# Kernel optimization log

Hardware: AMD Instinct MI355X
Metric: run time of the kernel (lower is better)

The kernel has to match this reference:

```python
import jax, jax.numpy as jnp
import numpy as np

B, S, DIM, H = 2, 2048, 1024, 16
DK = DIM // H  # 64
NEG = -10000000000.0


def setup_inputs() -> dict:
    key = jax.random.key(0)
    k1, k2, k3, k4, k5, k6 = jax.random.split(key, 6)
    dec_xs = jax.random.normal(k1, (B, S, DIM), dtype=jnp.float32)
    enc_xs = jax.random.normal(k2, (B, S, DIM), dtype=jnp.float32)
    mask = jax.random.randint(k3, (B, S, S), 0, 2, dtype=jnp.int32)
    # torch Linear weights: out = x @ W.T, bias=False
    sc = 1.0 / np.sqrt(DIM)
    Wq = jax.random.normal(k4, (DIM, DIM), dtype=jnp.float32) * sc
    Wkv = jax.random.normal(k5, (2 * DIM, DIM), dtype=jnp.float32) * sc
    Wo = jax.random.normal(k6, (DIM, DIM), dtype=jnp.float32) * sc
    return {"dec_xs": dec_xs, "enc_xs": enc_xs, "Wq": Wq, "Wkv": Wkv, "Wo": Wo, "mask": mask}


def reference(dec_xs, enc_xs, Wq, Wkv, Wo, mask):
    b, s, dim = enc_xs.shape
    qs = dec_xs @ Wq.T                      # [b,s,dim]  (dropout inactive in eval)
    kv = enc_xs @ Wkv.T                     # [b,s,2*dim]
    ks, vs = jnp.split(kv, 2, axis=-1)
    # head layout: view(b, s, dk, h) -- heads LAST, as in the original
    qs = qs.reshape(b, s, DK, H)
    ks = ks.reshape(b, s, DK, H)
    vs = vs.reshape(b, s, DK, H)
    scores = jnp.einsum('bqdh,bkdh->bqkh', qs, ks) / np.sqrt(DK)
    scores = jnp.where(mask[..., None] == 0, NEG, scores)
    weights = jax.nn.softmax(scores, axis=-2)  # softmax over key axis
    out = jnp.einsum('bqkh,bkdh->bqdh', weights, vs).reshape(b, s, dim)
    return out @ Wo.T
```

## Files before the change

kernel.cpp:

```cpp
#include <hip/hip_runtime.h>
#include <hip/hip_bf16.h>

#define BB 2
#define SS 2048
#define DIMM 1024
#define HH 16
#define DKK 64
#define QSCALE 0.18033688011112042592f

using bf16 = __hip_bfloat16;
typedef __attribute__((ext_vector_type(8))) short v8s;
typedef __attribute__((ext_vector_type(4))) short v4s;
typedef __attribute__((ext_vector_type(4))) float f32x4;
typedef __attribute__((ext_vector_type(16))) float f32x16;

using lds_u32 = __attribute__((address_space(3))) unsigned int;
using glb_u32 = const __attribute__((address_space(1))) unsigned int;

__device__ __forceinline__ void gload16(void* lds, const void* g) {
  __builtin_amdgcn_global_load_lds((glb_u32*)g, (lds_u32*)lds, 16, 0, 0);
}

__device__ __forceinline__ void cvt4(const float* __restrict__ s,
                                     bf16* __restrict__ d, int idx) {
  const float4 f = ((const float4*)s)[idx];
  bf16 t[4] = {__float2bfloat16(f.x), __float2bfloat16(f.y),
               __float2bfloat16(f.z), __float2bfloat16(f.w)};
  *(v4s*)(d + (size_t)idx * 4) = *(const v4s*)t;
}

__device__ __forceinline__ int cvt_pk_bf16(float lo, float hi) {
  int r;
  asm("v_cvt_pk_bf16_f32 %0, %1, %2" : "=v"(r) : "v"(lo), "v"(hi));
  return r;
}

__global__ __launch_bounds__(256) void convert_pack_kernel(
    const float* __restrict__ dec, const float* __restrict__ enc,
    const float* __restrict__ Wq, const float* __restrict__ Wkv,
    const float* __restrict__ Wo, const int* __restrict__ mask,
    bf16* __restrict__ decb, bf16* __restrict__ encb, bf16* __restrict__ Wqb,
    bf16* __restrict__ Wkvb, bf16* __restrict__ Wob,
    unsigned long long* __restrict__ mp) {
  const int gid = blockIdx.x * 256 + threadIdx.x;
  const int NT = 256 * 1024;
#pragma unroll
  for (int i = 0; i < 4; ++i) cvt4(dec, decb, gid + i * NT);
#pragma unroll
  for (int i = 0; i < 4; ++i) cvt4(enc, encb, gid + i * NT);
  cvt4(Wq, Wqb, gid);
#pragma unroll
  for (int i = 0; i < 2; ++i) cvt4(Wkv, Wkvb, gid + i * NT);
  {
    const int n = gid >> 8;
    const int c4 = (gid & 255) * 4;
    const int h = c4 >> 6, d0 = c4 & 63;
    const float* src = Wo + (size_t)n * DIMM + h;
    bf16 t[4];
#pragma unroll
    for (int i2 = 0; i2 < 4; ++i2)
      t[i2] = __float2bfloat16(src[(d0 + i2) * 16]);
    *(v4s*)(Wob + (size_t)n * DIMM + c4) = *(const v4s*)t;
  }
  const int lane = threadIdx.x & 63;
  const int wave_id = gid >> 6;
  for (int i = 0; i < 32; ++i) {
    const size_t w = (size_t)wave_id * 32 + i;
    const unsigned long long bm = __ballot(mask[w * 64 + lane] != 0);
    if (lane == 0) {
      const int bb = (int)(w >> 16);
      const int qq = (int)((w >> 5) & 2047);
      const int kc = (int)(w & 31);
      mp[((size_t)bb * 32 + kc) * SS + qq] = bm;
    }
  }
}

__global__ __launch_bounds__(256) void proj_gemm_kernel(
    const bf16* __restrict__ decb, const bf16* __restrict__ encb,
    const bf16* __restrict__ Wqb, const bf16* __restrict__ Wkvb,
    bf16* __restrict__ Qr, bf16* __restrict__ Kr, bf16* __restrict__ Vt) {
  __shared__ __align__(16) bf16 As[2][128][64];
  __shared__ __align__(16) bf16 Bs[2][128][64];
  const int t = threadIdx.x;
  const int wave = t >> 6, lane = t & 63;
  const int quad = lane >> 4, l15 = lane & 15;
  const int wm = (wave >> 1) * 64, wn = (wave & 1) * 64;

  const int bid = blockIdx.x;
  const int xcd = bid & 7, slot = bid >> 3;
  const int km = xcd + 8 * (slot >> 3);
  const int g = slot & 7;
  const int kind = km >> 5;
  const int m0 = (km & 31) * 128;

  const int lrow = lane >> 3;
  const int lcol = (lane & 7) * 8;

  const bf16* aptr[4];
  const bf16* bptr[4];
#pragma unroll
  for (int j = 0; j < 4; ++j) {
    const int r = (wave * 4 + j) * 8 + lrow;
    const int pw = (r & 63) * 16 + g * 2 + (r >> 6);
    if (kind == 0) {
      aptr[j] = decb + (size_t)(m0 + r) * DIMM + lcol;
      bptr[j] = Wqb + (size_t)pw * DIMM + lcol;
    } else if (kind == 1) {
      aptr[j] = encb + (size_t)(m0 + r) * DIMM + lcol;
      bptr[j] = Wkvb + (size_t)pw * DIMM + lcol;
    } else {
      aptr[j] = Wkvb + (size_t)(pw + DIMM) * DIMM + lcol;
      bptr[j] = encb + (size_t)(m0 + r) * DIMM + lcol;
    }
  }

  auto stage = [&](int kc, int buf) {
#pragma unroll
    for (int j = 0; j < 4; ++j) {
      gload16(&As[buf][(wave * 4 + j) * 8][0], aptr[j] + kc);
      gload16(&Bs[buf][(wave * 4 + j) * 8][0], bptr[j] + kc);
    }
  };

  f32x4 acc[4][4] = {};
  stage(0, 0);

  for (int kt = 0; kt < 16; ++kt) {
    const int cb = kt & 1;
    __syncthreads();
    if (kt < 15) stage((kt + 1) * 64, cb ^ 1);
#pragma unroll
    for (int ks = 0; ks < 2; ++ks) {
      v8s af[4], bfr[4];
#pragma unroll
      for (int i = 0; i < 4; ++i)
        af[i] = *(const v8s*)&As[cb][wm + i * 16 + l15][ks * 32 + quad * 8];
#pragma unroll
      for (int j = 0; j < 4; ++j)
        bfr[j] = *(const v8s*)&Bs[cb][wn + j * 16 + l15][ks * 32 + quad * 8];
#pragma unroll
      for (int i = 0; i < 4; ++i)
#pragma unroll
        for (int j = 0; j < 4; ++j)
          acc[i][j] = __builtin_amdgcn_mfma_f32_16x16x32_bf16(
              af[i], bfr[j], acc[i][j], 0, 0, 0);
    }
  }

#pragma unroll
  for (int i = 0; i < 4; ++i) {
#pragma unroll
    for (int r = 0; r < 4; ++r) {
      const int mm = wm + i * 16 + quad * 4 + r;
#pragma unroll
      for (int j = 0; j < 4; ++j) {
        const int nn = wn + j * 16 + l15;
        const float v = acc[i][j][r];
        if (kind == 0) {
          Qr[(size_t)(m0 + mm) * DIMM + g * 128 + nn] =
              __float2bfloat16(v * QSCALE);
        } else if (kind == 1) {
          Kr[(size_t)(m0 + mm) * DIMM + g * 128 + nn] = __float2bfloat16(v);
        } else {
          const int h = g * 2 + (mm >> 6), d = mm & 63;
          const int sn = m0 + nn;
          const int b = sn >> 11, s = sn & (SS - 1);
          Vt[(((size_t)b * HH + h) * DKK + d) * SS + s] = __float2bfloat16(v);
        }
      }
    }
  }
}

__global__ __launch_bounds__(256) void out_gemm_kernel(
    const bf16* __restrict__ A, const bf16* __restrict__ W,
    float* __restrict__ out) {
  __shared__ __align__(16) bf16 As[2][128][64];
  __shared__ __align__(16) bf16 Bs[2][128][64];
  const int t = threadIdx.x;
  const int wave = t >> 6, lane = t & 63;
  const int quad = lane >> 4, l15 = lane & 15;
  const int wm = (wave >> 1) * 64, wn = (wave & 1) * 64;

  const int bid = blockIdx.x;
  const int xcd = bid & 7, slot = bid >> 3;
  const int m0 = (xcd + 8 * (slot >> 3)) * 128;
  const int n0 = (slot & 7) * 128;

  const int lrow = lane >> 3;
  const int lcol = (lane & 7) * 8;

  const bf16* aptr[4];
  const bf16* bptr[4];
#pragma unroll
  for (int j = 0; j < 4; ++j) {
    const int r = (wave * 4 + j) * 8 + lrow;
    aptr[j] = A + (size_t)(m0 + r) * DIMM + lcol;
    bptr[j] = W + (size_t)(n0 + r) * DIMM + lcol;
  }

  auto stage = [&](int kc, int buf) {
#pragma unroll
    for (int j = 0; j < 4; ++j) {
      gload16(&As[buf][(wave * 4 + j) * 8][0], aptr[j] + kc);
      gload16(&Bs[buf][(wave * 4 + j) * 8][0], bptr[j] + kc);
    }
  };

  f32x4 acc[4][4] = {};
  stage(0, 0);

  for (int kt = 0; kt < 16; ++kt) {
    const int cb = kt & 1;
    __syncthreads();
    if (kt < 15) stage((kt + 1) * 64, cb ^ 1);
#pragma unroll
    for (int ks = 0; ks < 2; ++ks) {
      v8s af[4], bfr[4];
#pragma unroll
      for (int i = 0; i < 4; ++i)
        af[i] = *(const v8s*)&As[cb][wm + i * 16 + l15][ks * 32 + quad * 8];
#pragma unroll
      for (int j = 0; j < 4; ++j)
        bfr[j] = *(const v8s*)&Bs[cb][wn + j * 16 + l15][ks * 32 + quad * 8];
#pragma unroll
      for (int i = 0; i < 4; ++i)
#pragma unroll
        for (int j = 0; j < 4; ++j)
          acc[i][j] = __builtin_amdgcn_mfma_f32_16x16x32_bf16(
              af[i], bfr[j], acc[i][j], 0, 0, 0);
    }
  }

#pragma unroll
  for (int i = 0; i < 4; ++i) {
#pragma unroll
    for (int r = 0; r < 4; ++r) {
      const int m = m0 + wm + i * 16 + quad * 4 + r;
#pragma unroll
      for (int j = 0; j < 4; ++j) {
        const int n = n0 + wn + j * 16 + l15;
        out[(size_t)m * DIMM + n] = acc[i][j][r];
      }
    }
  }
}

__global__ __launch_bounds__(512) void attn_kernel(
    const bf16* __restrict__ Qr, const bf16* __restrict__ Kr,
    const bf16* __restrict__ Vt, const unsigned long long* __restrict__ mp,
    bf16* __restrict__ Ar) {
  __shared__ __align__(16) bf16 smem[2][2][2][64][72];

  const int t = threadIdx.x;
  const int wave = t >> 6, lane = t & 63;
  const int l31 = lane & 31, hf = lane >> 5;
  const int qb = wave & 3;
  const int pr = wave >> 2;

  const int bx = blockIdx.x;
  const int xcd = bx & 7, j = bx >> 3;
  const int g = (xcd << 2) | (j & 3);
  const int tile = j >> 2;
  const int hd = g & 15, b = g >> 4;

  const int qw = tile * 128 + qb * 32;
  const size_t bhv = ((size_t)b * HH + hd) * DKK;

  v8s bq[4];
  {
    const bf16* qrow = Qr + ((size_t)(b * SS + qw + l31)) * DIMM + hd * 64;
#pragma unroll
    for (int cs = 0; cs < 4; ++cs)
      bq[cs] = *(const v8s*)(qrow + cs * 16 + 8 * hf);
  }

  v8s vones;
#pragma unroll
  for (int i = 0; i < 8; ++i) vones[i] = (short)0x3F80;

  f32x16 o0 = {}, o1 = {}, ol = {};

  const int r0 = t >> 3;
  const int c0 = (t & 7) * 8;

  auto gK = [&](int kt) {
    return *(const v8s*)(Kr + ((size_t)(b * SS + kt * 64 + r0)) * DIMM +
                         hd * 64 + c0);
  };
  auto gV = [&](int kt) {
    return *(const v8s*)(Vt + (bhv + r0) * SS + kt * 64 + c0);
  };
  auto loadM = [&](int kt) {
    return mp[((size_t)b * 32 + kt) * SS + qw + l31];
  };

  {
    const v8s k0 = gK(0), v0 = gV(0), k1 = gK(1), v1 = gV(1);
    *(v8s*)&smem[0][0][0][r0][c0] = k0;
    *(v8s*)&smem[1][0][0][r0][c0] = v0;
    *(v8s*)&smem[0][1][0][r0][c0] = k1;
    *(v8s*)&smem[1][1][0][r0][c0] = v1;
  }
  v8s kpr[2], vpr[2];
  kpr[0] = gK(2);
  vpr[0] = gV(2);
  kpr[1] = gK(3);
  vpr[1] = gV(3);
  unsigned long long mwcur = loadM(pr);

  for (int s = 0; s < 16; ++s) {
    __syncthreads();
    const int nb = (s + 1) & 1;
    if (s < 15) {
      *(v8s*)&smem[0][0][nb][r0][c0] = kpr[0];
      *(v8s*)&smem[1][0][nb][r0][c0] = vpr[0];
      *(v8s*)&smem[0][1][nb][r0][c0] = kpr[1];
      *(v8s*)&smem[1][1][nb][r0][c0] = vpr[1];
      if (s < 14) {
        kpr[0] = gK(2 * s + 4);
        vpr[0] = gV(2 * s + 4);
        kpr[1] = gK(2 * s + 5);
        vpr[1] = gV(2 * s + 5);
      }
    }
    const unsigned long long mwnext = (s < 15) ? loadM(2 * s + 2 + pr) : 0ULL;
    const unsigned long long mq = mwcur >> (4 * hf);
    const int cb = s & 1;

    f32x16 st[2];
#pragma unroll
    for (int n = 0; n < 2; ++n) {
      f32x16 sa = {};
#pragma unroll
      for (int cs = 0; cs < 4; ++cs) {
        const v8s ak =
            *(const v8s*)&smem[0][pr][cb][n * 32 + l31][cs * 16 + 8 * hf];
        sa = __builtin_amdgcn_mfma_f32_32x32x16_bf16(ak, bq[cs], sa, 0, 0, 0);
      }
      st[n] = sa;
    }

    int pd[8][2];
#pragma unroll
    for (int n = 0; n < 2; ++n)
#pragma unroll
      for (int g2 = 0; g2 < 4; ++g2)
#pragma unroll
        for (int jj = 0; jj < 2; ++jj) {
          const int bp = 32 * n + 8 * g2 + 2 * jj;
          const int m = g2 * 4 + 2 * jj;
          const float p0 =
              ((mq >> bp) & 1) ? __builtin_amdgcn_exp2f(st[n][m]) : 0.f;
          const float p1 =
              ((mq >> (bp + 1)) & 1) ? __builtin_amdgcn_exp2f(st[n][m + 1])
                                     : 0.f;
          pd[n * 4 + g2][jj] = cvt_pk_bf16(p0, p1);
        }

    v8s af[4];
#pragma unroll
    for (int ks = 0; ks < 4; ++ks) {
      int a0 = pd[2 * ks][0], b0 = pd[2 * ks + 1][0];
      int a1 = pd[2 * ks][1], b1 = pd[2 * ks + 1][1];
      asm("v_permlane32_swap_b32 %0, %1" : "+v"(a0), "+v"(b0));
      asm("v_permlane32_swap_b32 %0, %1" : "+v"(a1), "+v"(b1));
      int4 w;
      w.x = a0;
      w.y = a1;
      w.z = b0;
      w.w = b1;
      af[ks] = *(v8s*)&w;
    }

#pragma unroll
    for (int ks = 0; ks < 4; ++ks) {
      const v8s bv0 = *(const v8s*)&smem[1][pr][cb][l31][ks * 16 + 8 * hf];
      const v8s bv1 =
          *(const v8s*)&smem[1][pr][cb][32 + l31][ks * 16 + 8 * hf];
      o0 = __builtin_amdgcn_mfma_f32_32x32x16_bf16(af[ks], bv0, o0, 0, 0, 0);
      o1 = __builtin_amdgcn_mfma_f32_32x32x16_bf16(af[ks], bv1, o1, 0, 0, 0);
      ol = __builtin_amdgcn_mfma_f32_32x32x16_bf16(af[ks], vones, ol, 0, 0, 0);
    }
    mwcur = mwnext;
  }

  __syncthreads();
  float* scratch = (float*)&smem[0][0][0][0][0];
  if (wave >= 4) {
    float* dst = scratch + ((size_t)(wave - 4) * 64 + lane) * 52;
#pragma unroll
    for (int i = 0; i < 4; ++i) {
      f32x4 t0 = {o0[4 * i], o0[4 * i + 1], o0[4 * i + 2], o0[4 * i + 3]};
      f32x4 t1 = {o1[4 * i], o1[4 * i + 1], o1[4 * i + 2], o1[4 * i + 3]};
      f32x4 t2 = {ol[4 * i], ol[4 * i + 1], ol[4 * i + 2], ol[4 * i + 3]};
      *(f32x4*)(dst + 4 * i) = t0;
      *(f32x4*)(dst + 16 + 4 * i) = t1;
      *(f32x4*)(dst + 32 + 4 * i) = t2;
    }
  }
  __syncthreads();
  if (wave < 4) {
    const float* src = scratch + ((size_t)wave * 64 + lane) * 52;
#pragma unroll
    for (int m = 0; m < 16; ++m) {
      o0[m] += src[m];
      o1[m] += src[16 + m];
      ol[m] += src[32 + m];
    }
#pragma unroll
    for (int m = 0; m < 16; ++m) {
      const float inv = __builtin_amdgcn_rcpf(ol[m]);
      const int q = qw + (m & 3) + 8 * (m >> 2) + 4 * hf;
      const size_t row = (size_t)b * SS + q;
      Ar[row * DIMM + hd * 64 + l31] = __float2bfloat16(o0[m] * inv);
      Ar[row * DIMM + hd * 64 + 32 + l31] = __float2bfloat16(o1[m] * inv);
    }
  }
}

extern "C" void kernel_launch(void* const* d_in, const int* in_sizes, int n_in,
                              void* d_out, int out_size, void* d_ws,
                              size_t ws_size, hipStream_t stream) {
  const float* dec = (const float*)d_in[0];
  const float* enc = (const float*)d_in[1];
  const float* Wq = (const float*)d_in[2];
  const float* Wkv = (const float*)d_in[3];
  const float* Wo = (const float*)d_in[4];
  const int* mask = (const int*)d_in[5];
  float* out = (float*)d_out;

  bf16* decb = (bf16*)d_out;
  bf16* Wqb = (bf16*)((char*)d_out + ((size_t)2 * SS * DIMM * 2));

  char* ws = (char*)d_ws;
  size_t off = 0;
  bf16* encb = (bf16*)(ws + off);
  bf16* Ar = (bf16*)(ws + off);   off += (size_t)2 * SS * DIMM * 2;
  bf16* Wkvb = (bf16*)(ws + off); off += (size_t)2 * DIMM * DIMM * 2;
  bf16* Wob = (bf16*)(ws + off);  off += (size_t)DIMM * DIMM * 2;
  bf16* Qr = (bf16*)(ws + off);   off += (size_t)2 * SS * DIMM * 2;
  bf16* Kr = (bf16*)(ws + off);   off += (size_t)2 * SS * DIMM * 2;
  bf16* Vt = (bf16*)(ws + off);   off += (size_t)2 * SS * DIMM * 2;
  unsigned long long* mp = (unsigned long long*)(ws + off);

  dim3 blk(256);
  convert_pack_kernel<<<dim3(1024), blk, 0, stream>>>(
      dec, enc, Wq, Wkv, Wo, mask, decb, encb, Wqb, Wkvb, Wob, mp);
  proj_gemm_kernel<<<dim3(768), blk, 0, stream>>>(decb, encb, Wqb, Wkvb, Qr,
                                                  Kr, Vt);
  attn_kernel<<<dim3(512), dim3(512), 0, stream>>>(Qr, Kr, Vt, mp, Ar);
  out_gemm_kernel<<<dim3(256), blk, 0, stream>>>(Ar, Wob, out);
}
```

Before: 268.2 us.

## Swizzle proj GEMM LDS layout and retile output GEMM to 128x64 padded tiles

Result: faster. 242.4 us (-9.6%).

```diff
diff --git a/kernel.cpp b/kernel.cpp
--- a/kernel.cpp
+++ b/kernel.cpp
@@ -95,7 +95,7 @@
   const int m0 = (km & 31) * 128;
 
   const int lrow = lane >> 3;
-  const int lcol = (lane & 7) * 8;
+  const int lcol = ((lane & 7) ^ lrow) * 8;
 
   const bf16* aptr[4];
   const bf16* bptr[4];
@@ -132,13 +132,14 @@
     if (kt < 15) stage((kt + 1) * 64, cb ^ 1);
 #pragma unroll
     for (int ks = 0; ks < 2; ++ks) {
+      const int rc = (((ks * 4 + quad) ^ (l15 & 7)) * 8);
       v8s af[4], bfr[4];
 #pragma unroll
       for (int i = 0; i < 4; ++i)
-        af[i] = *(const v8s*)&As[cb][wm + i * 16 + l15][ks * 32 + quad * 8];
+        af[i] = *(const v8s*)&As[cb][wm + i * 16 + l15][rc];
 #pragma unroll
       for (int j = 0; j < 4; ++j)
-        bfr[j] = *(const v8s*)&Bs[cb][wn + j * 16 + l15][ks * 32 + quad * 8];
+        bfr[j] = *(const v8s*)&Bs[cb][wn + j * 16 + l15][rc];
 #pragma unroll
       for (int i = 0; i < 4; ++i)
 #pragma unroll
@@ -176,58 +177,66 @@
 __global__ __launch_bounds__(256) void out_gemm_kernel(
     const bf16* __restrict__ A, const bf16* __restrict__ W,
     float* __restrict__ out) {
-  __shared__ __align__(16) bf16 As[2][128][64];
-  __shared__ __align__(16) bf16 Bs[2][128][64];
+  __shared__ __align__(16) bf16 As[128][72];
+  __shared__ __align__(16) bf16 Bs[64][72];
   const int t = threadIdx.x;
   const int wave = t >> 6, lane = t & 63;
   const int quad = lane >> 4, l15 = lane & 15;
-  const int wm = (wave >> 1) * 64, wn = (wave & 1) * 64;
+  const int wm = (wave >> 1) * 64, wn = (wave & 1) * 32;
 
   const int bid = blockIdx.x;
   const int xcd = bid & 7, slot = bid >> 3;
-  const int m0 = (xcd + 8 * (slot >> 3)) * 128;
-  const int n0 = (slot & 7) * 128;
-
-  const int lrow = lane >> 3;
-  const int lcol = (lane & 7) * 8;
-
-  const bf16* aptr[4];
-  const bf16* bptr[4];
-#pragma unroll
-  for (int j = 0; j < 4; ++j) {
-    const int r = (wave * 4 + j) * 8 + lrow;
-    aptr[j] = A + (size_t)(m0 + r) * DIMM + lcol;
-    bptr[j] = W + (size_t)(n0 + r) * DIMM + lcol;
-  }
-
-  auto stage = [&](int kc, int buf) {
-#pragma unroll
-    for (int j = 0; j < 4; ++j) {
-      gload16(&As[buf][(wave * 4 + j) * 8][0], aptr[j] + kc);
-      gload16(&Bs[buf][(wave * 4 + j) * 8][0], bptr[j] + kc);
-    }
-  };
-
-  f32x4 acc[4][4] = {};
-  stage(0, 0);
-
-  for (int kt = 0; kt < 16; ++kt) {
-    const int cb = kt & 1;
+  const int m0 = (xcd + 8 * (slot >> 4)) * 128;
+  const int n0 = (slot & 15) * 64;
+
+  const int sr = t >> 2;
+  const int sc = (t & 3) * 16;
+
+  v8s ar[4], br[2];
+  auto loadA = [&](int kc) {
+#pragma unroll
+    for (int rr = 0; rr < 2; ++rr) {
+      const bf16* p = A + (size_t)(m0 + sr + rr * 64) * DIMM + kc + sc;
+#pragma unroll
+      for (int i = 0; i < 2; ++i) ar[rr * 2 + i] = ((const v8s*)p)[i];
+    }
+  };
+  auto loadB = [&](int kc) {
+    const bf16* p = W + (size_t)(n0 + sr) * DIMM + kc + sc;
+#pragma unroll
+    for (int i = 0; i < 2; ++i) br[i] = ((const v8s*)p)[i];
+  };
+
+  f32x4 acc[4][2] = {};
+  loadA(0);
+  loadB(0);
+  for (int kc = 0; kc < DIMM; kc += 64) {
     __syncthreads();
-    if (kt < 15) stage((kt + 1) * 64, cb ^ 1);
+#pragma unroll
+    for (int rr = 0; rr < 2; ++rr) {
+      *(v8s*)&As[sr + rr * 64][sc] = ar[rr * 2 + 0];
+      *(v8s*)&As[sr + rr * 64][sc + 8] = ar[rr * 2 + 1];
+    }
+    *(v8s*)&Bs[sr][sc] = br[0];
+    *(v8s*)&Bs[sr][sc + 8] = br[1];
+    if (kc + 64 < DIMM) {
+      loadA(kc + 64);
+      loadB(kc + 64);
+    }
+    __syncthreads();
 #pragma unroll
     for (int ks = 0; ks < 2; ++ks) {
-      v8s af[4], bfr[4];
+      v8s af[4], bfr[2];
 #pragma unroll
       for (int i = 0; i < 4; ++i)
-        af[i] = *(const v8s*)&As[cb][wm + i * 16 + l15][ks * 32 + quad * 8];
-#pragma unroll
-      for (int j = 0; j < 4; ++j)
-        bfr[j] = *(const v8s*)&Bs[cb][wn + j * 16 + l15][ks * 32 + quad * 8];
+        af[i] = *(const v8s*)&As[wm + i * 16 + l15][ks * 32 + quad * 8];
+#pragma unroll
+      for (int j = 0; j < 2; ++j)
+        bfr[j] = *(const v8s*)&Bs[wn + j * 16 + l15][ks * 32 + quad * 8];
 #pragma unroll
       for (int i = 0; i < 4; ++i)
 #pragma unroll
-        for (int j = 0; j < 4; ++j)
+        for (int j = 0; j < 2; ++j)
           acc[i][j] = __builtin_amdgcn_mfma_f32_16x16x32_bf16(
               af[i], bfr[j], acc[i][j], 0, 0, 0);
     }
@@ -239,7 +248,7 @@
     for (int r = 0; r < 4; ++r) {
       const int m = m0 + wm + i * 16 + quad * 4 + r;
 #pragma unroll
-      for (int j = 0; j < 4; ++j) {
+      for (int j = 0; j < 2; ++j) {
         const int n = n0 + wn + j * 16 + l15;
         out[(size_t)m * DIMM + n] = acc[i][j][r];
       }
@@ -451,5 +460,5 @@
   proj_gemm_kernel<<<dim3(768), blk, 0, stream>>>(decb, encb, Wqb, Wkvb, Qr,
                                                   Kr, Vt);
   attn_kernel<<<dim3(512), dim3(512), 0, stream>>>(Qr, Kr, Vt, mp, Ar);
-  out_gemm_kernel<<<dim3(256), blk, 0, stream>>>(Ar, Wob, out);
-}
+  out_gemm_kernel<<<dim3(512), blk, 0, stream>>>(Ar, Wob, out);
+}
```
